# Optimization experiments

Hardware: AMD Instinct MI355X
Metric: run time of the kernel (lower is better)

The kernel has to match this reference:

```python
import jax, jax.numpy as jnp
import numpy as np

NB = 10   # num_boxes
NC = 14   # num_classes
LC = 19   # channels per anchor: conf, x, y, w, h + NC classes
N_OBJ = 256


def _split(t):
    # t: [B, NB*LC, H, W] -> (conf, x, y, w, h), each [B, NB, H, W]
    return tuple(t[:, i:NB * LC + i:LC] for i in range(5))


def _iou_corners(b1, b2):
    # b1, b2: [..., 4] as (x1, y1, x2, y2)
    x1 = jnp.maximum(b1[..., 0], b2[..., 0])
    y1 = jnp.maximum(b1[..., 1], b2[..., 1])
    x2 = jnp.minimum(b1[..., 2], b2[..., 2])
    y2 = jnp.minimum(b1[..., 3], b2[..., 3])
    inter = jnp.clip(x2 - x1, 0.0) * jnp.clip(y2 - y1, 0.0)
    a1 = jnp.abs((b1[..., 2] - b1[..., 0]) * (b1[..., 3] - b1[..., 1]))
    a2 = jnp.abs((b2[..., 2] - b2[..., 0]) * (b2[..., 3] - b2[..., 1]))
    return inter / (a1 + a2 - inter + 1e-6)


def _responsible_anchor(pred_boxes, target_boxes, grids):
    # Faithful port of YOLOLoss.IOUcalc including its sequential integer state
    # and the quirky membership row max_IOU[b][:][h][w] == max_IOU[b, h, w, :].
    B, _, H, W, _ = pred_boxes.shape
    b, g, h, w = grids[:, 0], grids[:, 1], grids[:, 2], grids[:, 3]
    tb = target_boxes[b, g, h, w]                 # [N, 4]
    pb = pred_boxes[b, :, h, w]                   # [N, NB, 4]
    ious = jax.lax.stop_gradient(_iou_corners(tb[:, None, :], pb))  # [N, NB]
    maxI0 = jnp.zeros((B, NB, H, W), jnp.int32)

    def step(mI, inp):
        grid, iou_row = inp
        gb, gg, gh, gw = grid[0], grid[1], grid[2], grid[3]

        def anchor(a, mI):
            cur = mI[gb, gg, gh, gw]
            row = mI[gb, gh, gw, :]  # torch quirk: anchor dim indexed by h, H dim by w
            cond = (cur.astype(iou_row.dtype) < iou_row[a]) & jnp.all(row != a)
            return mI.at[gb, gg, gh, gw].set(jnp.where(cond, a, cur))

        return jax.lax.fori_loop(0, NB, anchor, mI), None

    maxI, _ = jax.lax.scan(step, maxI0, (grids, ious))
    return maxI


def _yolo_loss(predictions, targets, valid_grids,
               lambda_coord=5.0, lambda_noobj=5.0, lambda_loc=7.0):
    tc, tx, ty, tw, th = _split(targets)
    pc, px, py, pw, ph = _split(predictions)
    # corner-format boxes [B, NB, H, W, 4]
    pb = jnp.stack((px - pw / 2, py - ph / 2, px + pw / 2, py + ph / 2), -1)
    tb = jnp.stack((tx - tw / 2, ty - th / 2, tx + tw / 2, ty + th / 2), -1)
    maxI = _responsible_anchor(pb, tb, valid_grids)

    b, g, h, w = valid_grids[:, 0], valid_grids[:, 1], valid_grids[:, 2], valid_grids[:, 3]
    sel = maxI[b, g, h, w]       # responsible anchor for w/h/conf/class terms
    sel_xy = maxI[b, g, h, h]    # original bug: grids[2] used twice for x/y terms
    n = valid_grids.shape[0]

    x_l = (tx[b, g, h, w] - px[b, sel_xy, h, w]) ** 2
    y_l = (ty[b, g, h, w] - py[b, sel_xy, h, w]) ** 2
    w_l = (jnp.sqrt(jnp.clip(tw[b, g, h, w], 0.0)) - jnp.sqrt(jnp.clip(pw[b, sel, h, w], 0.0))) ** 2
    h_l = (jnp.sqrt(jnp.clip(th[b, g, h, w], 0.0)) - jnp.sqrt(jnp.clip(ph[b, sel, h, w], 0.0))) ** 2
    localization = jnp.sum(x_l + y_l + w_l + h_l) / n

    conf_obj = jnp.sum((tc[b, g, h, w] - pc[b, sel, h, w]) ** 2) / n

    conf_nothing = ((tc - pc) ** 2).at[b, sel, h, w].set(0.0).mean()

    cls_off = jnp.arange(NC)
    p_cls = predictions[b[:, None], (sel * LC + 5)[:, None] + cls_off, h[:, None], w[:, None]]  # [N, NC]
    t_cls = targets[b[:, None], (b * LC + 5)[:, None] + cls_off, h[:, None], w[:, None]]        # original bug: b*19
    class_loss = jnp.sum(jnp.mean((p_cls - t_cls) ** 2, axis=1)) / n

    return (lambda_loc * localization + lambda_coord * conf_obj
            + lambda_noobj * conf_nothing + class_loss)


def setup_inputs() -> dict:
    key = jax.random.key(0)
    B, H, W = 8, 96, 96
    C = NB * LC
    k1, k2, k3 = jax.random.split(key, 3)
    predictions = jax.random.uniform(k1, (B, C, H, W), jnp.float32)
    targets = jax.random.uniform(k2, (B, C, H, W), jnp.float32)
    targets = targets.at[:, 0:C:LC].set(0.0)  # confidence zero everywhere
    # 256 unique object cells; quirky-indexing constraints: b < 10, h < NB, H == W
    H_OBJ = 10
    rng = np.random.default_rng(0)
    flat = rng.choice(B * NB * H_OBJ * W, size=N_OBJ, replace=False)
    gb, r = np.divmod(flat, NB * H_OBJ * W)
    gg, r = np.divmod(r, H_OBJ * W)
    gh, gw = np.divmod(r, W)
    grids = np.stack([gb, gg, gh, gw], axis=1)
    grids = grids[np.lexsort((gw, gh, gg, gb))]  # torch.unique(dim=0) sorts rows
    valid_grids = jnp.asarray(grids, jnp.int32)
    conf = jax.random.uniform(k3, (N_OBJ,), jnp.float32, minval=0.3, maxval=1.0)
    targets = targets.at[valid_grids[:, 0], valid_grids[:, 1] * LC,
                         valid_grids[:, 2], valid_grids[:, 3]].set(conf)
    return {"predictions": predictions, "targets": targets, "valid_grids": valid_grids}


def reference(predictions, targets, valid_grids):
    return _yolo_loss(predictions, targets, valid_grids)
```

## Files before the change

kernel.cpp:

```cpp
#include <hip/hip_runtime.h>

#define NBANCH 10
#define NCLS   14
#define LCH    19
#define NOBJ   256
#define BBATCH 8
#define HH     96
#define WW     96
#define NCHTOT 190
#define PLANE  (HH*WW)
#define TOTCONF (BBATCH*NBANCH*PLANE)
#define NCONFBLK 720

__device__ __forceinline__ float ldat(const float* __restrict__ p, int b, int c, int hw) {
    return p[(size_t)(b * NCHTOT + c) * PLANE + hw];
}

#define IOU_OFF 0
#define XY_OFF  2560
#define WH_OFF  5120
#define CO_OFF  7680
#define CLS_OFF 10240
#define SUB_OFF 12800

__global__ __launch_bounds__(256) void fused_pre(const float* __restrict__ pred,
                                                 const float* __restrict__ targ,
                                                 const int* __restrict__ grids,
                                                 double* __restrict__ conf_part,
                                                 float* __restrict__ gw) {
    if (blockIdx.x < NCONFBLK) {
        int tid = blockIdx.x * 256 + threadIdx.x;
        int plane = tid / 2304;
        int r = tid - plane * 2304;
        int b = plane / NBANCH;
        int g = plane - b * NBANCH;
        size_t off = (size_t)(b * NCHTOT + g * LCH) * PLANE + (size_t)r * 4;
        float4 t4 = *reinterpret_cast<const float4*>(targ + off);
        float4 p4 = *reinterpret_cast<const float4*>(pred + off);
        float dx = t4.x - p4.x, dy = t4.y - p4.y, dz = t4.z - p4.z, dw = t4.w - p4.w;
        double s = (double)(dx*dx) + (double)(dy*dy) + (double)(dz*dz) + (double)(dw*dw);
        for (int o = 32; o > 0; o >>= 1) s += __shfl_down(s, o, 64);
        __shared__ double wsum[4];
        int lane = threadIdx.x & 63, wid = threadIdx.x >> 6;
        if (lane == 0) wsum[wid] = s;
        __syncthreads();
        if (threadIdx.x == 0) conf_part[blockIdx.x] = wsum[0] + wsum[1] + wsum[2] + wsum[3];
        return;
    }

    int gi = blockIdx.x - NCONFBLK;
    int a = threadIdx.x;
    if (a >= NBANCH) return;
    const int b = grids[gi*4+0], g = grids[gi*4+1], h = grids[gi*4+2], w = grids[gi*4+3];
    const int hw = h * WW + w;

    const float tc = ldat(targ, b, g*LCH+0, hw);
    const float tx = ldat(targ, b, g*LCH+1, hw);
    const float ty = ldat(targ, b, g*LCH+2, hw);
    const float tw = ldat(targ, b, g*LCH+3, hw);
    const float th = ldat(targ, b, g*LCH+4, hw);
    const float tb0 = tx - tw*0.5f, tb1 = ty - th*0.5f;
    const float tb2 = tx + tw*0.5f, tb3 = ty + th*0.5f;
    const float ta  = fabsf((tb2 - tb0) * (tb3 - tb1));

    const float pc = ldat(pred, b, a*LCH+0, hw);
    const float px = ldat(pred, b, a*LCH+1, hw);
    const float py = ldat(pred, b, a*LCH+2, hw);
    const float pw = ldat(pred, b, a*LCH+3, hw);
    const float ph = ldat(pred, b, a*LCH+4, hw);
    const float tca = ldat(targ, b, a*LCH+0, hw);

    const float pb0 = px - pw*0.5f, pb1 = py - ph*0.5f;
    const float pb2 = px + pw*0.5f, pb3 = py + ph*0.5f;
    float x1 = fmaxf(tb0, pb0), y1 = fmaxf(tb1, pb1);
    float x2 = fminf(tb2, pb2), y2 = fminf(tb3, pb3);
    float inter = fmaxf(x2 - x1, 0.f) * fmaxf(y2 - y1, 0.f);
    float pa = fabsf((pb2 - pb0) * (pb3 - pb1));
    float iou = inter / (((ta + pa) - inter) + 1e-6f);

    float dxl = tx - px, dyl = ty - py;
    float xy  = dxl*dxl + dyl*dyl;
    float dwl = sqrtf(fmaxf(tw, 0.f)) - sqrtf(fmaxf(pw, 0.f));
    float dhl = sqrtf(fmaxf(th, 0.f)) - sqrtf(fmaxf(ph, 0.f));
    float wh  = dwl*dwl + dhl*dhl;
    float dco = tc - pc;
    float co  = dco*dco;
    float dsb = tca - pc;
    float sub = dsb*dsb;

    float clsf = 0.f;
    #pragma unroll
    for (int c = 0; c < NCLS; ++c) {
        float d = ldat(pred, b, a*LCH+5+c, hw) - ldat(targ, b, b*LCH+5+c, hw);
        clsf += d * d;
    }
    float cls = clsf / 14.f;

    int idx = gi * NBANCH + a;
    gw[IOU_OFF + idx] = iou;
    gw[XY_OFF  + idx] = xy;
    gw[WH_OFF  + idx] = wh;
    gw[CO_OFF  + idx] = co;
    gw[CLS_OFF + idx] = cls;
    gw[SUB_OFF + idx] = sub;
}

__global__ __launch_bounds__(256) void yolo_main(const int* __restrict__ grids,
                                                 const double* __restrict__ conf_part,
                                                 const float* __restrict__ gw,
                                                 float* __restrict__ out) {
    __shared__ int packed[NOBJ];
    __shared__ int sels[NOBJ];
    __shared__ int keys[NOBJ];
    __shared__ int changed;
    __shared__ double wpart[4][5];

    const int i = threadIdx.x;
    const int b = grids[i*4+0], g = grids[i*4+1], h = grids[i*4+2], w = grids[i*4+3];
    packed[i] = (b << 24) | (g << 16) | (h << 8) | w;

    float iou_r[NBANCH];
    int afirst = 0;
    #pragma unroll
    for (int a = 0; a < NBANCH; ++a) {
        float v = gw[IOU_OFF + i*NBANCH + a];
        iou_r[a] = v;
        if (a >= 1 && afirst == 0 && v > 0.f) afirst = a;
    }
    sels[i] = afirst;
    if (i == 0) changed = 0;
    __syncthreads();

    const int mkey = (b << 16) | (h << 8) | w;
    unsigned long long m0 = 0, m1 = 0, m2 = 0, m3 = 0;
    #pragma unroll 8
    for (int j = 0; j < 64; ++j)
        m0 |= ((unsigned long long)((packed[j] >> 8) == mkey)) << j;
    #pragma unroll 8
    for (int j = 64; j < 128; ++j)
        m1 |= ((unsigned long long)((packed[j] >> 8) == mkey)) << (j - 64);
    #pragma unroll 8
    for (int j = 128; j < 192; ++j)
        m2 |= ((unsigned long long)((packed[j] >> 8) == mkey)) << (j - 128);
    #pragma unroll 8
    for (int j = 192; j < 256; ++j)
        m3 |= ((unsigned long long)((packed[j] >> 8) == mkey)) << (j - 192);

    const bool selfin = ((i < 64 ? m0 : i < 128 ? m1 : i < 192 ? m2 : m3) >> (i & 63)) & 1ull;
    unsigned long long w0 = m0, w1 = m1, w2 = m2, w3 = m3;
    if (i < 64)       w0 &= ~(1ull << i);
    else if (i < 128) w1 &= ~(1ull << (i - 64));
    else if (i < 192) w2 &= ~(1ull << (i - 128));
    else              w3 &= ~(1ull << (i - 192));

    const bool inS = (m0 | m1 | m2 | m3) != 0ull;
    const int kc = __popcll(m0) + __popcll(m1) + __popcll(m2) + __popcll(m3);

    for (int round = 0; round < NOBJ; ++round) {
        int nv = sels[i];
        if (inS) {
            int present = selfin ? 1 : 0;
            unsigned long long mm;
            mm = w0; while (mm) { int j = __ffsll((long long)mm) - 1;       mm &= mm - 1; present |= 1 << ((j < i) ? sels[j] : 0); }
            mm = w1; while (mm) { int j = 64  + __ffsll((long long)mm) - 1; mm &= mm - 1; present |= 1 << ((j < i) ? sels[j] : 0); }
            mm = w2; while (mm) { int j = 128 + __ffsll((long long)mm) - 1; mm &= mm - 1; present |= 1 << ((j < i) ? sels[j] : 0); }
            mm = w3; while (mm) { int j = 192 + __ffsll((long long)mm) - 1; mm &= mm - 1; present |= 1 << ((j < i) ? sels[j] : 0); }
            int cur = 0;
            #pragma unroll
            for (int a = 0; a < NBANCH; ++a) {
                if ((float)cur < iou_r[a]) {
                    bool ok = ((a != 0) || (kc == 96)) && !((present >> a) & 1);
                    if (ok) cur = a;
                }
            }
            nv = cur;
        }
        __syncthreads();
        if (inS && nv != sels[i]) { sels[i] = nv; changed = 1; }
        __syncthreads();
        int c = changed;
        __syncthreads();
        if (i == 0) changed = 0;
        if (!c) break;
    }

    const int sel = sels[i];
    const int pkxy = (b << 24) | (g << 16) | (h << 8) | h;
    int sxy = 0;
    #pragma unroll 8
    for (int j = 0; j < NOBJ; ++j) {
        bool m = (packed[j] == pkxy);
        int v = sels[j];
        sxy = m ? v : sxy;
    }

    keys[i] = ((b * NBANCH + sel) * HH + h) * WW + w;
    __syncthreads();
    const int myk = keys[i];
    int dup = 0;
    #pragma unroll 8
    for (int j = 0; j < NOBJ; ++j) {
        dup |= (int)((j < i) & (keys[j] == myk));
    }
    const bool firstocc = (dup == 0);

    double loc = (double)gw[XY_OFF + i*NBANCH + sxy] + (double)gw[WH_OFF + i*NBANCH + sel];
    double co  = (double)gw[CO_OFF + i*NBANCH + sel];
    double cls = (double)gw[CLS_OFF + i*NBANCH + sel];
    double sub = firstocc ? (double)gw[SUB_OFF + i*NBANCH + sel] : 0.0;

    double cp = conf_part[i];
    if (i + 256 < NCONFBLK) cp += conf_part[i + 256];
    if (i + 512 < NCONFBLK) cp += conf_part[i + 512];

    double v0 = loc, v1 = co, v2 = cls, v3 = sub, v4 = cp;
    #pragma unroll
    for (int o = 32; o > 0; o >>= 1) {
        v0 += __shfl_down(v0, o, 64);
        v1 += __shfl_down(v1, o, 64);
        v2 += __shfl_down(v2, o, 64);
        v3 += __shfl_down(v3, o, 64);
        v4 += __shfl_down(v4, o, 64);
    }
    const int lane = i & 63, wid = i >> 6;
    if (lane == 0) {
        wpart[wid][0] = v0; wpart[wid][1] = v1; wpart[wid][2] = v2;
        wpart[wid][3] = v3; wpart[wid][4] = v4;
    }
    __syncthreads();
    if (i == 0) {
        double s0 = 0, s1 = 0, s2 = 0, s3 = 0, s4 = 0;
        #pragma unroll
        for (int k = 0; k < 4; ++k) {
            s0 += wpart[k][0]; s1 += wpart[k][1]; s2 += wpart[k][2];
            s3 += wpart[k][3]; s4 += wpart[k][4];
        }
        double locS = s0 / 256.0;
        double coS  = s1 / 256.0;
        double clsS = s2 / 256.0;
        double cn   = (s4 - s3) / (double)TOTCONF;
        out[0] = (float)(7.0 * locS + 5.0 * coS + 5.0 * cn + clsS);
    }
}

extern "C" void kernel_launch(void* const* d_in, const int* in_sizes, int n_in,
                              void* d_out, int out_size, void* d_ws, size_t ws_size,
                              hipStream_t stream) {
    const float* pred = (const float*)d_in[0];
    const float* targ = (const float*)d_in[1];
    const int*  grids = (const int*)d_in[2];
    float* out = (float*)d_out;
    double* conf_part = (double*)d_ws;
    float* gw = (float*)((char*)d_ws + NCONFBLK * sizeof(double));

    fused_pre<<<NCONFBLK + NOBJ, 256, 0, stream>>>(pred, targ, grids, conf_part, gw);
    yolo_main<<<1, 256, 0, stream>>>(grids, conf_part, gw, out);
}
```

Measured before the change: 132.3 us.

## Fuse pre-pass and final reduction into one kernel via last-block atomic counter

Merges the two kernels into one. The last block to finish, found with an atomic counter and thread fences, runs the sequential anchor-assignment and reduction. The confidence sum now has each thread process four float4 pairs over 180 blocks instead of 720. The per-object gather packs 2560 (object, anchor) pairs densely into 10 full blocks instead of 256 mostly idle blocks. This removes one kernel launch boundary and many idle waves, but adds a memset launch and the cost of the atomic and fences.

```diff
diff --git a/kernel.cpp b/kernel.cpp
--- a/kernel.cpp
+++ b/kernel.cpp
@@ -10,7 +10,10 @@
 #define NCHTOT 190
 #define PLANE  (HH*WW)
 #define TOTCONF (BBATCH*NBANCH*PLANE)
-#define NCONFBLK 720
+
+#define NCONFBLK 180
+#define NGATHBLK 10
+#define NBLK (NCONFBLK + NGATHBLK)
 
 __device__ __forceinline__ float ldat(const float* __restrict__ p, int b, int c, int hw) {
     return p[(size_t)(b * NCHTOT + c) * PLANE + hw];
@@ -22,100 +25,113 @@
 #define CO_OFF  7680
 #define CLS_OFF 10240
 #define SUB_OFF 12800
-
-__global__ __launch_bounds__(256) void fused_pre(const float* __restrict__ pred,
-                                                 const float* __restrict__ targ,
-                                                 const int* __restrict__ grids,
-                                                 double* __restrict__ conf_part,
-                                                 float* __restrict__ gw) {
+#define CNT_BYTE_OFF 65536
+
+__global__ __launch_bounds__(256) void yolo_fused(const float* __restrict__ pred,
+                                                  const float* __restrict__ targ,
+                                                  const int* __restrict__ grids,
+                                                  double* __restrict__ conf_part,
+                                                  float* __restrict__ gw,
+                                                  unsigned int* __restrict__ counter,
+                                                  float* __restrict__ out) {
+    __shared__ double wsum[4];
+    __shared__ int finish;
+
+    const int tid = threadIdx.x;
+
     if (blockIdx.x < NCONFBLK) {
-        int tid = blockIdx.x * 256 + threadIdx.x;
-        int plane = tid / 2304;
-        int r = tid - plane * 2304;
-        int b = plane / NBANCH;
-        int g = plane - b * NBANCH;
-        size_t off = (size_t)(b * NCHTOT + g * LCH) * PLANE + (size_t)r * 4;
-        float4 t4 = *reinterpret_cast<const float4*>(targ + off);
-        float4 p4 = *reinterpret_cast<const float4*>(pred + off);
-        float dx = t4.x - p4.x, dy = t4.y - p4.y, dz = t4.z - p4.z, dw = t4.w - p4.w;
-        double s = (double)(dx*dx) + (double)(dy*dy) + (double)(dz*dz) + (double)(dw*dw);
+        int base = blockIdx.x * 256 + tid;
+        double s = 0.0;
+        #pragma unroll
+        for (int k = 0; k < 4; ++k) {
+            int f = base + k * (NCONFBLK * 256);
+            int plane = f / 2304;
+            int r = f - plane * 2304;
+            int b = plane / NBANCH;
+            int g = plane - b * NBANCH;
+            size_t off = (size_t)(b * NCHTOT + g * LCH) * PLANE + (size_t)r * 4;
+            float4 t4 = *reinterpret_cast<const float4*>(targ + off);
+            float4 p4 = *reinterpret_cast<const float4*>(pred + off);
+            float dx = t4.x - p4.x, dy = t4.y - p4.y, dz = t4.z - p4.z, dw = t4.w - p4.w;
+            s += (double)(dx*dx) + (double)(dy*dy) + (double)(dz*dz) + (double)(dw*dw);
+        }
+        #pragma unroll
         for (int o = 32; o > 0; o >>= 1) s += __shfl_down(s, o, 64);
-        __shared__ double wsum[4];
-        int lane = threadIdx.x & 63, wid = threadIdx.x >> 6;
-        if (lane == 0) wsum[wid] = s;
-        __syncthreads();
-        if (threadIdx.x == 0) conf_part[blockIdx.x] = wsum[0] + wsum[1] + wsum[2] + wsum[3];
-        return;
-    }
-
-    int gi = blockIdx.x - NCONFBLK;
-    int a = threadIdx.x;
-    if (a >= NBANCH) return;
-    const int b = grids[gi*4+0], g = grids[gi*4+1], h = grids[gi*4+2], w = grids[gi*4+3];
-    const int hw = h * WW + w;
-
-    const float tc = ldat(targ, b, g*LCH+0, hw);
-    const float tx = ldat(targ, b, g*LCH+1, hw);
-    const float ty = ldat(targ, b, g*LCH+2, hw);
-    const float tw = ldat(targ, b, g*LCH+3, hw);
-    const float th = ldat(targ, b, g*LCH+4, hw);
-    const float tb0 = tx - tw*0.5f, tb1 = ty - th*0.5f;
-    const float tb2 = tx + tw*0.5f, tb3 = ty + th*0.5f;
-    const float ta  = fabsf((tb2 - tb0) * (tb3 - tb1));
-
-    const float pc = ldat(pred, b, a*LCH+0, hw);
-    const float px = ldat(pred, b, a*LCH+1, hw);
-    const float py = ldat(pred, b, a*LCH+2, hw);
-    const float pw = ldat(pred, b, a*LCH+3, hw);
-    const float ph = ldat(pred, b, a*LCH+4, hw);
-    const float tca = ldat(targ, b, a*LCH+0, hw);
-
-    const float pb0 = px - pw*0.5f, pb1 = py - ph*0.5f;
-    const float pb2 = px + pw*0.5f, pb3 = py + ph*0.5f;
-    float x1 = fmaxf(tb0, pb0), y1 = fmaxf(tb1, pb1);
-    float x2 = fminf(tb2, pb2), y2 = fminf(tb3, pb3);
-    float inter = fmaxf(x2 - x1, 0.f) * fmaxf(y2 - y1, 0.f);
-    float pa = fabsf((pb2 - pb0) * (pb3 - pb1));
-    float iou = inter / (((ta + pa) - inter) + 1e-6f);
-
-    float dxl = tx - px, dyl = ty - py;
-    float xy  = dxl*dxl + dyl*dyl;
-    float dwl = sqrtf(fmaxf(tw, 0.f)) - sqrtf(fmaxf(pw, 0.f));
-    float dhl = sqrtf(fmaxf(th, 0.f)) - sqrtf(fmaxf(ph, 0.f));
-    float wh  = dwl*dwl + dhl*dhl;
-    float dco = tc - pc;
-    float co  = dco*dco;
-    float dsb = tca - pc;
-    float sub = dsb*dsb;
-
-    float clsf = 0.f;
-    #pragma unroll
-    for (int c = 0; c < NCLS; ++c) {
-        float d = ldat(pred, b, a*LCH+5+c, hw) - ldat(targ, b, b*LCH+5+c, hw);
-        clsf += d * d;
-    }
-    float cls = clsf / 14.f;
-
-    int idx = gi * NBANCH + a;
-    gw[IOU_OFF + idx] = iou;
-    gw[XY_OFF  + idx] = xy;
-    gw[WH_OFF  + idx] = wh;
-    gw[CO_OFF  + idx] = co;
-    gw[CLS_OFF + idx] = cls;
-    gw[SUB_OFF + idx] = sub;
-}
-
-__global__ __launch_bounds__(256) void yolo_main(const int* __restrict__ grids,
-                                                 const double* __restrict__ conf_part,
-                                                 const float* __restrict__ gw,
-                                                 float* __restrict__ out) {
+        if ((tid & 63) == 0) wsum[tid >> 6] = s;
+        __syncthreads();
+        if (tid == 0) conf_part[blockIdx.x] = wsum[0] + wsum[1] + wsum[2] + wsum[3];
+    } else {
+        int pair = (blockIdx.x - NCONFBLK) * 256 + tid;
+        int gi = pair / NBANCH;
+        int a  = pair - gi * NBANCH;
+        const int b = grids[gi*4+0], g = grids[gi*4+1], h = grids[gi*4+2], w = grids[gi*4+3];
+        const int hw = h * WW + w;
+
+        const float tc = ldat(targ, b, g*LCH+0, hw);
+        const float tx = ldat(targ, b, g*LCH+1, hw);
+        const float ty = ldat(targ, b, g*LCH+2, hw);
+        const float tw = ldat(targ, b, g*LCH+3, hw);
+        const float th = ldat(targ, b, g*LCH+4, hw);
+        const float tb0 = tx - tw*0.5f, tb1 = ty - th*0.5f;
+        const float tb2 = tx + tw*0.5f, tb3 = ty + th*0.5f;
+        const float ta  = fabsf((tb2 - tb0) * (tb3 - tb1));
+
+        const float pc = ldat(pred, b, a*LCH+0, hw);
+        const float px = ldat(pred, b, a*LCH+1, hw);
+        const float py = ldat(pred, b, a*LCH+2, hw);
+        const float pw = ldat(pred, b, a*LCH+3, hw);
+        const float ph = ldat(pred, b, a*LCH+4, hw);
+        const float tca = ldat(targ, b, a*LCH+0, hw);
+
+        const float pb0 = px - pw*0.5f, pb1 = py - ph*0.5f;
+        const float pb2 = px + pw*0.5f, pb3 = py + ph*0.5f;
+        float x1 = fmaxf(tb0, pb0), y1 = fmaxf(tb1, pb1);
+        float x2 = fminf(tb2, pb2), y2 = fminf(tb3, pb3);
+        float inter = fmaxf(x2 - x1, 0.f) * fmaxf(y2 - y1, 0.f);
+        float pa = fabsf((pb2 - pb0) * (pb3 - pb1));
+        float iou = inter / (((ta + pa) - inter) + 1e-6f);
+
+        float dxl = tx - px, dyl = ty - py;
+        float xy  = dxl*dxl + dyl*dyl;
+        float dwl = sqrtf(fmaxf(tw, 0.f)) - sqrtf(fmaxf(pw, 0.f));
+        float dhl = sqrtf(fmaxf(th, 0.f)) - sqrtf(fmaxf(ph, 0.f));
+        float wh  = dwl*dwl + dhl*dhl;
+        float dco = tc - pc;
+        float dsb = tca - pc;
+
+        float clsf = 0.f;
+        #pragma unroll
+        for (int c = 0; c < NCLS; ++c) {
+            float d = ldat(pred, b, a*LCH+5+c, hw) - ldat(targ, b, b*LCH+5+c, hw);
+            clsf += d * d;
+        }
+
+        int idx = gi * NBANCH + a;
+        gw[IOU_OFF + idx] = iou;
+        gw[XY_OFF  + idx] = xy;
+        gw[WH_OFF  + idx] = wh;
+        gw[CO_OFF  + idx] = dco * dco;
+        gw[CLS_OFF + idx] = clsf / 14.f;
+        gw[SUB_OFF + idx] = dsb * dsb;
+    }
+
+    __threadfence();
+    __syncthreads();
+    if (tid == 0) {
+        unsigned int old = atomicAdd(counter, 1u);
+        finish = (old == NBLK - 1) ? 1 : 0;
+    }
+    __syncthreads();
+    if (!finish) return;
+    __threadfence();
+
     __shared__ int packed[NOBJ];
     __shared__ int sels[NOBJ];
     __shared__ int keys[NOBJ];
     __shared__ int changed;
     __shared__ double wpart[4][5];
 
-    const int i = threadIdx.x;
+    const int i = tid;
     const int b = grids[i*4+0], g = grids[i*4+1], h = grids[i*4+2], w = grids[i*4+3];
     packed[i] = (b << 24) | (g << 16) | (h << 8) | w;
 
@@ -208,10 +224,7 @@
     double co  = (double)gw[CO_OFF + i*NBANCH + sel];
     double cls = (double)gw[CLS_OFF + i*NBANCH + sel];
     double sub = firstocc ? (double)gw[SUB_OFF + i*NBANCH + sel] : 0.0;
-
-    double cp = conf_part[i];
-    if (i + 256 < NCONFBLK) cp += conf_part[i + 256];
-    if (i + 512 < NCONFBLK) cp += conf_part[i + 512];
+    double cp  = (i < NCONFBLK) ? conf_part[i] : 0.0;
 
     double v0 = loc, v1 = co, v2 = cls, v3 = sub, v4 = cp;
     #pragma unroll
@@ -252,7 +265,8 @@
     float* out = (float*)d_out;
     double* conf_part = (double*)d_ws;
     float* gw = (float*)((char*)d_ws + NCONFBLK * sizeof(double));
-
-    fused_pre<<<NCONFBLK + NOBJ, 256, 0, stream>>>(pred, targ, grids, conf_part, gw);
-    yolo_main<<<1, 256, 0, stream>>>(grids, conf_part, gw, out);
+    unsigned int* counter = (unsigned int*)((char*)d_ws + CNT_BYTE_OFF);
+
+    hipMemsetAsync(counter, 0, sizeof(unsigned int), stream);
+    yolo_fused<<<NBLK, 256, 0, stream>>>(pred, targ, grids, conf_part, gw, counter, out);
 }
```

Result: slower. 157.5 us (+19.0%).
